# Optimization experiments

Measured on AMD Instinct MI355X. Metric: run time of the kernel, lower is better.

Reference implementation:

```python
import jax, jax.numpy as jnp
import numpy as np

# Mamba-1.4B-like dims
BATCH, SEQ, HID = 1, 2048, 2048
INTER, STATE, DT_RANK, KCONV = 4096, 16, 128, 4


def setup_inputs() -> dict:
    key = jax.random.key(0)
    ks = jax.random.split(key, 8)
    f = jnp.float32
    return {
        "input_states": jax.random.normal(ks[0], (BATCH, SEQ, HID), f),
        "in_proj_w": jax.random.normal(ks[1], (HID, 2 * INTER), f) * (HID ** -0.5),
        "conv_w": jax.random.normal(ks[2], (INTER, 1, KCONV), f) * (KCONV ** -0.5),  # (O, I/groups=1, K) depthwise
        "conv_b": jnp.zeros((INTER,), f),
        "x_proj_w": jax.random.normal(ks[3], (INTER, DT_RANK + 2 * STATE), f) * (INTER ** -0.5),
        "dt_proj_w": jax.random.normal(ks[4], (DT_RANK, INTER), f) * (DT_RANK ** -0.5),
        "dt_proj_b": jax.random.normal(ks[5], (INTER,), f) * 0.1,
        "A_log": jnp.log(jnp.broadcast_to(jnp.arange(1, STATE + 1, dtype=f), (INTER, STATE))),
        "D": jnp.ones((INTER,), f),
        "out_proj_w": jax.random.normal(ks[6], (INTER, HID), f) * (INTER ** -0.5),
    }


def _mamba_forward(input_states, in_proj_w, conv_w, conv_b, x_proj_w,
                   dt_proj_w, dt_proj_b, A_log, D, out_proj_w):
    Bsz, L, _ = input_states.shape
    Idim, _, K = conv_w.shape
    N = A_log.shape[1]
    R = dt_proj_w.shape[0]

    proj = input_states @ in_proj_w                       # (B, L, 2I)
    hidden, gate = jnp.split(proj, 2, axis=-1)            # each (B, L, I)

    # depthwise causal conv over sequence (pad K-1, keep first L outputs)
    xc = jnp.swapaxes(hidden, 1, 2)                       # (B, I, L)
    xc = jax.lax.conv_general_dilated(
        xc, conv_w, window_strides=(1,), padding=((K - 1, K - 1),),
        feature_group_count=Idim)
    xc = xc[:, :, :L] + conv_b[None, :, None]
    u = jax.nn.silu(jnp.swapaxes(xc, 1, 2))               # (B, L, I)

    # input-dependent SSM params
    ssm_in = u @ x_proj_w                                 # (B, L, R + 2N)
    dt_in, Bc, Cc = jnp.split(ssm_in, [R, R + N], axis=-1)
    dt = jax.nn.softplus(dt_in @ dt_proj_w + dt_proj_b)   # (B, L, I)
    A = -jnp.exp(A_log)                                   # (I, N)

    def step(state, xs):
        dt_t, B_t, C_t, u_t = xs                          # (B,I) (B,N) (B,N) (B,I)
        dA = jnp.exp(dt_t[:, :, None] * A[None])          # (B, I, N)
        state = state * dA + (dt_t * u_t)[:, :, None] * B_t[:, None, :]
        y_t = jnp.einsum('bin,bn->bi', state, C_t)
        return state, y_t

    xs = (jnp.swapaxes(dt, 0, 1), jnp.swapaxes(Bc, 0, 1),
          jnp.swapaxes(Cc, 0, 1), jnp.swapaxes(u, 0, 1))
    state0 = jnp.zeros((Bsz, Idim, N), dt.dtype)
    _, ys = jax.lax.scan(step, state0, xs)                # (L, B, I)
    y = jnp.swapaxes(ys, 0, 1)                            # (B, L, I)

    y = (y + u * D) * jax.nn.silu(gate)
    return y @ out_proj_w                                 # (B, L, H)


def reference(input_states, in_proj_w, conv_w, conv_b, x_proj_w,
              dt_proj_w, dt_proj_b, A_log, D, out_proj_w):
    return _mamba_forward(input_states, in_proj_w, conv_w, conv_b, x_proj_w,
                          dt_proj_w, dt_proj_b, A_log, D, out_proj_w)
```

## Files before the change

### kernel.cpp

```cpp
#include <hip/hip_runtime.h>
#include <stdint.h>

#define LSEQ 2048
#define HID  2048
#define IDIM 4096
#define NSTATE 16
#define RRANK 128
#define GDIM 160

#define GCHUNK 64
#define TCHUNK (LSEQ / GCHUNK)

typedef _Float16 f16x8 __attribute__((ext_vector_type(8)));
typedef _Float16 f16x2 __attribute__((ext_vector_type(2)));
typedef float f32x4 __attribute__((ext_vector_type(4)));

#define GLOAD_LDS16(g, l) __builtin_amdgcn_global_load_lds( \
    (const __attribute__((address_space(1))) void*)(g),     \
    (__attribute__((address_space(3))) void*)(l), 16, 0, 0)

__device__ __forceinline__ float softplus_f(float x) {
    if (x > 20.f) return x;
    return log1pf(__expf(x));
}
__device__ __forceinline__ float silu_f(float x) {
    return x / (1.f + __expf(-x));
}

__device__ __forceinline__ void transpose_tile(const float* __restrict__ in,
                                               _Float16* __restrict__ out,
                                               int R, int C, int tr, int tc,
                                               _Float16 (*tile)[66]) {
    const int c0 = tc * 64, r0 = tr * 64;
    const int t = threadIdx.x;
    const int tx = t & 15, ty = t >> 4;
    const int ox = t & 7, oy = t >> 3;
    const bool full = (c0 + 64 <= C) && (r0 + 64 <= R);
    if (full) {
        #pragma unroll
        for (int j = 0; j < 4; ++j) {
            int r = ty + j * 16;
            float4 v = *(const float4*)(in + (long)(r0 + r) * C + c0 + tx * 4);
            tile[r][tx * 4 + 0] = (_Float16)v.x;
            tile[r][tx * 4 + 1] = (_Float16)v.y;
            tile[r][tx * 4 + 2] = (_Float16)v.z;
            tile[r][tx * 4 + 3] = (_Float16)v.w;
        }
        __syncthreads();
        #pragma unroll
        for (int j = 0; j < 2; ++j) {
            int c = oy + j * 32;
            f16x8 v;
            #pragma unroll
            for (int e = 0; e < 8; ++e) v[e] = tile[ox * 8 + e][c];
            *(f16x8*)(out + (long)(c0 + c) * R + r0 + ox * 8) = v;
        }
    } else {
        #pragma unroll
        for (int j = 0; j < 4; ++j) {
            int r = ty + j * 16;
            #pragma unroll
            for (int e = 0; e < 4; ++e) {
                int c = c0 + tx * 4 + e;
                float v = (r0 + r < R && c < C) ? in[(long)(r0 + r) * C + c] : 0.f;
                tile[r][tx * 4 + e] = (_Float16)v;
            }
        }
        __syncthreads();
        #pragma unroll
        for (int j = 0; j < 2; ++j) {
            int c = c0 + oy + j * 32;
            if (c < C) {
                #pragma unroll
                for (int e = 0; e < 8; ++e) {
                    int r = r0 + ox * 8 + e;
                    if (r < R) out[(long)c * R + r] = tile[ox * 8 + e][oy + j * 32];
                }
            }
        }
    }
}

__global__ __launch_bounds__(256)
void prep_kernel(const float* __restrict__ x_in, const float* __restrict__ w_in,
                 const float* __restrict__ xw, const float* __restrict__ dtw,
                 const float* __restrict__ ow,
                 _Float16* __restrict__ Xf, _Float16* __restrict__ Wt1,
                 _Float16* __restrict__ Wt2, _Float16* __restrict__ Wt3,
                 _Float16* __restrict__ Wt4) {
    __shared__ _Float16 tile[64][66];
    int b = blockIdx.x;
    if (b < 4096) { transpose_tile(w_in, Wt1, HID, 2 * IDIM, b / 128, b % 128, tile); return; }
    b -= 4096;
    if (b < 192) { transpose_tile(xw, Wt2, IDIM, GDIM, b / 3, b % 3, tile); return; }
    b -= 192;
    if (b < 128) { transpose_tile(dtw, Wt3, RRANK, IDIM, b / 64, b % 64, tile); return; }
    b -= 128;
    if (b < 2048) { transpose_tile(ow, Wt4, IDIM, HID, b / 32, b % 32, tile); return; }
    b -= 2048;
    long base = (long)b * 4096 + threadIdx.x * 16;
    #pragma unroll
    for (int h = 0; h < 2; ++h) {
        float4 a = *(const float4*)(x_in + base + h * 8);
        float4 c = *(const float4*)(x_in + base + h * 8 + 4);
        f16x8 v;
        v[0] = (_Float16)a.x; v[1] = (_Float16)a.y; v[2] = (_Float16)a.z; v[3] = (_Float16)a.w;
        v[4] = (_Float16)c.x; v[5] = (_Float16)c.y; v[6] = (_Float16)c.z; v[7] = (_Float16)c.w;
        *(f16x8*)(Xf + base + h * 8) = v;
    }
}

#define BM 128
#define BK 64

template <typename CT, int BN_, bool SOFTPLUS>
__global__ __launch_bounds__(256)
void gemm_bt_kernel(const _Float16* __restrict__ A, const _Float16* __restrict__ Bt,
                    CT* __restrict__ C, int M, int N, int K, int kc,
                    const float* __restrict__ bias) {
    constexpr int NI = BN_ / 32;
    constexpr int NISS_B = BN_ * 8 / 256;
    __shared__ _Float16 As[BM * BK];
    __shared__ _Float16 Bs[BN_ * BK];
    const int m0 = blockIdx.y * BM;
    const int n0 = blockIdx.x * BN_;
    const int t = threadIdx.x;
    const int wave = t >> 6;
    const int lane = t & 63;
    const int wm = wave >> 1, wn = wave & 1;
    const int lrow = lane & 15;
    const int quad = lane >> 4;
    const int sw8 = (lrow & 7) * 8;

    f32x4 acc[4][NI];
    #pragma unroll
    for (int mi = 0; mi < 4; ++mi)
        #pragma unroll
        for (int ni = 0; ni < NI; ++ni)
            #pragma unroll
            for (int r = 0; r < 4; ++r)
                acc[mi][ni][r] = 0.f;

    const int k_begin = blockIdx.z * kc;
    const _Float16* pA[4];
    #pragma unroll
    for (int j = 0; j < 4; ++j) {
        int s = j * 256 + t;
        int row = s >> 3;
        int ch = (s & 7) ^ (row & 7);
        pA[j] = A + (long)(m0 + row) * K + ch * 8 + k_begin;
    }
    const _Float16* pB[NISS_B];
    #pragma unroll
    for (int j = 0; j < NISS_B; ++j) {
        int s = j * 256 + t;
        int row = s >> 3;
        int ch = (s & 7) ^ (row & 7);
        pB[j] = Bt + (long)(n0 + row) * K + ch * 8 + k_begin;
    }

    for (int kk = 0; kk < kc; kk += BK) {
        #pragma unroll
        for (int j = 0; j < 4; ++j) {
            GLOAD_LDS16(pA[j], As + (j * 256 + wave * 64) * 8);
            pA[j] += BK;
        }
        #pragma unroll
        for (int j = 0; j < NISS_B; ++j) {
            GLOAD_LDS16(pB[j], Bs + (j * 256 + wave * 64) * 8);
            pB[j] += BK;
        }
        __syncthreads();

        #pragma unroll
        for (int h = 0; h < 2; ++h) {
            const int qoff = (h * 32 + quad * 8) ^ sw8;
            f16x8 af[4], bf[NI];
            #pragma unroll
            for (int mi = 0; mi < 4; ++mi)
                af[mi] = *(const f16x8*)(As + (wm * 64 + mi * 16 + lrow) * BK + qoff);
            #pragma unroll
            for (int ni = 0; ni < NI; ++ni)
                bf[ni] = *(const f16x8*)(Bs + (wn * (BN_ / 2) + ni * 16 + lrow) * BK + qoff);
            #pragma unroll
            for (int mi = 0; mi < 4; ++mi)
                #pragma unroll
                for (int ni = 0; ni < NI; ++ni)
                    acc[mi][ni] = __builtin_amdgcn_mfma_f32_16x16x32_f16(af[mi], bf[ni], acc[mi][ni], 0, 0, 0);
        }
        __syncthreads();
    }

    CT* Cz = C + (long)blockIdx.z * M * N;
    #pragma unroll
    for (int mi = 0; mi < 4; ++mi) {
        #pragma unroll
        for (int ni = 0; ni < NI; ++ni) {
            int col = n0 + wn * (BN_ / 2) + ni * 16 + lrow;
            if (col < N) {
                float bv = SOFTPLUS ? bias[col] : 0.f;
                #pragma unroll
                for (int r = 0; r < 4; ++r) {
                    int row = m0 + wm * 64 + mi * 16 + quad * 4 + r;
                    float v = acc[mi][ni][r];
                    if (SOFTPLUS) v = softplus_f(v + bv);
                    Cz[(long)row * N + col] = (CT)v;
                }
            }
        }
    }
}

__global__ void xproj_reduce_kernel(const float* __restrict__ part, float* __restrict__ ssm,
                                    _Float16* __restrict__ dtin) {
    int idx = blockIdx.x * 256 + threadIdx.x;
    if (idx >= LSEQ * GDIM) return;
    int t = idx / GDIM;
    int c = idx - t * GDIM;
    float v = 0.f;
    #pragma unroll
    for (int k = 0; k < 8; ++k)
        v += part[((long)k * LSEQ + t) * 256 + c];
    ssm[idx] = v;
    if (c < RRANK) dtin[t * RRANK + c] = (_Float16)v;
}

__global__ void opart_reduce_kernel(const float* __restrict__ part, float* __restrict__ out) {
    int idx = blockIdx.x * 256 + threadIdx.x;
    float4 a = ((const float4*)part)[idx];
    float4 b = ((const float4*)(part + (long)LSEQ * HID))[idx];
    ((float4*)out)[idx] = make_float4(a.x + b.x, a.y + b.y, a.z + b.z, a.w + b.w);
}

__global__ void conv_silu_kernel(const _Float16* __restrict__ proj, const float* __restrict__ w,
                                 const float* __restrict__ b, _Float16* __restrict__ u16) {
    int idx = blockIdx.x * 256 + threadIdx.x;
    int i0 = (idx & 511) * 8;
    int t0 = (idx >> 9) * 4;
    f16x8 r[7];
    #pragma unroll
    for (int k = 0; k < 7; ++k) {
        int tt = t0 - 3 + k;
        if (tt >= 0) r[k] = *(const f16x8*)(proj + (long)tt * (2 * IDIM) + i0);
        else         r[k] = f16x8{0,0,0,0,0,0,0,0};
    }
    float4 wv[8]; float bb[8];
    #pragma unroll
    for (int j = 0; j < 8; ++j) { wv[j] = ((const float4*)w)[i0 + j]; bb[j] = b[i0 + j]; }
    #pragma unroll
    for (int tt = 0; tt < 4; ++tt) {
        f16x8 res;
        #pragma unroll
        for (int j = 0; j < 8; ++j) {
            float a = bb[j] + (float)r[tt][j] * wv[j].x + (float)r[tt+1][j] * wv[j].y
                            + (float)r[tt+2][j] * wv[j].z + (float)r[tt+3][j] * wv[j].w;
            res[j] = (_Float16)(a / (1.f + __expf(-a)));
        }
        *(f16x8*)(u16 + (long)(t0 + tt) * IDIM + i0) = res;
    }
}

__global__ __launch_bounds__(256)
void scan_pass1_kernel(const _Float16* __restrict__ dtf, const float* __restrict__ ssm,
                       const _Float16* __restrict__ u16, const float* __restrict__ A_log,
                       _Float16* __restrict__ Pc, _Float16* __restrict__ Sc) {
    const int c = blockIdx.y;
    const int i0 = (blockIdx.x * 256 + threadIdx.x) * 2;

    __shared__ float Bs[TCHUNK * 16];
    for (int idx = threadIdx.x; idx < TCHUNK * 16; idx += 256) {
        int t = idx >> 4, n = idx & 15;
        Bs[idx] = ssm[(c * TCHUNK + t) * GDIM + RRANK + n];
    }
    __syncthreads();

    float A[2][16];
    #pragma unroll
    for (int ch = 0; ch < 2; ++ch) {
        const float4* Ap = (const float4*)(A_log + (long)(i0 + ch) * 16);
        #pragma unroll
        for (int q = 0; q < 4; ++q) {
            float4 v = Ap[q];
            A[ch][q * 4 + 0] = -__expf(v.x);
            A[ch][q * 4 + 1] = -__expf(v.y);
            A[ch][q * 4 + 2] = -__expf(v.z);
            A[ch][q * 4 + 3] = -__expf(v.w);
        }
    }

    float s[2][16], pr[2][16];
    #pragma unroll
    for (int ch = 0; ch < 2; ++ch)
        #pragma unroll
        for (int n = 0; n < 16; ++n) { s[ch][n] = 0.f; pr[ch][n] = 1.f; }

    long base = (long)c * TCHUNK * IDIM + i0;
    for (int t = 0; t < TCHUNK; ++t) {
        f16x2 dt2 = *(const f16x2*)(dtf + base + (long)t * IDIM);
        f16x2 u2  = *(const f16x2*)(u16 + base + (long)t * IDIM);
        #pragma unroll
        for (int ch = 0; ch < 2; ++ch) {
            float dt = (float)dt2[ch];
            float dtu = dt * (float)u2[ch];
            #pragma unroll
            for (int n = 0; n < 16; ++n) {
                float dA = __expf(dt * A[ch][n]);
                s[ch][n] = s[ch][n] * dA + dtu * Bs[t * 16 + n];
                pr[ch][n] *= dA;
            }
        }
    }

    long o = ((long)c * IDIM + i0) * 16;
    #pragma unroll
    for (int ch = 0; ch < 2; ++ch) {
        #pragma unroll
        for (int q = 0; q < 2; ++q) {
            f16x8 pv, sv;
            #pragma unroll
            for (int e = 0; e < 8; ++e) {
                pv[e] = (_Float16)pr[ch][q * 8 + e];
                sv[e] = (_Float16)s[ch][q * 8 + e];
            }
            *(f16x8*)(Pc + o + ch * 16 + q * 8) = pv;
            *(f16x8*)(Sc + o + ch * 16 + q * 8) = sv;
        }
    }
}

__global__ void scan_combine_kernel(const _Float16* __restrict__ Pc, _Float16* __restrict__ ScInit) {
    int tid = blockIdx.x * 256 + threadIdx.x;
    const long stride = (long)IDIM * 16;
    const long off = (long)tid * 2;
    f16x2 p4[4], s4[4];
    #pragma unroll
    for (int k = 0; k < 4; ++k) {
        p4[k] = *(const f16x2*)(Pc + (long)k * stride + off);
        s4[k] = *(const f16x2*)(ScInit + (long)k * stride + off);
    }
    float c0 = 0.f, c1 = 0.f;
    for (int g = 0; g < GCHUNK / 4; ++g) {
        f16x2 pc[4], sc[4];
        #pragma unroll
        for (int k = 0; k < 4; ++k) { pc[k] = p4[k]; sc[k] = s4[k]; }
        if (g + 1 < GCHUNK / 4) {
            #pragma unroll
            for (int k = 0; k < 4; ++k) {
                long o2 = (long)((g + 1) * 4 + k) * stride + off;
                p4[k] = *(const f16x2*)(Pc + o2);
                s4[k] = *(const f16x2*)(ScInit + o2);
            }
        }
        #pragma unroll
        for (int k = 0; k < 4; ++k) {
            long o = (long)(g * 4 + k) * stride + off;
            *(f16x2*)(ScInit + o) = f16x2{(_Float16)c0, (_Float16)c1};
            c0 = c0 * (float)pc[k][0] + (float)sc[k][0];
            c1 = c1 * (float)pc[k][1] + (float)sc[k][1];
        }
    }
}

__global__ __launch_bounds__(256)
void scan_pass3_kernel(const _Float16* __restrict__ dtf, const float* __restrict__ ssm,
                       const _Float16* __restrict__ u16, const _Float16* __restrict__ proj,
                       const float* __restrict__ A_log, const float* __restrict__ Dp,
                       const _Float16* __restrict__ Init, _Float16* __restrict__ y16) {
    const int c = blockIdx.y;
    const int i0 = (blockIdx.x * 256 + threadIdx.x) * 2;

    __shared__ float Bs[TCHUNK * 16];
    __shared__ float Cs[TCHUNK * 16];
    for (int idx = threadIdx.x; idx < TCHUNK * 16; idx += 256) {
        int t = idx >> 4, n = idx & 15;
        Bs[idx] = ssm[(c * TCHUNK + t) * GDIM + RRANK + n];
        Cs[idx] = ssm[(c * TCHUNK + t) * GDIM + RRANK + NSTATE + n];
    }
    __syncthreads();

    float A[2][16];
    #pragma unroll
    for (int ch = 0; ch < 2; ++ch) {
        const float4* Ap = (const float4*)(A_log + (long)(i0 + ch) * 16);
        #pragma unroll
        for (int q = 0; q < 4; ++q) {
            float4 v = Ap[q];
            A[ch][q * 4 + 0] = -__expf(v.x);
            A[ch][q * 4 + 1] = -__expf(v.y);
            A[ch][q * 4 + 2] = -__expf(v.z);
            A[ch][q * 4 + 3] = -__expf(v.w);
        }
    }
    float2 Dv = *(const float2*)(Dp + i0);

    float s[2][16];
    {
        long o = ((long)c * IDIM + i0) * 16;
        #pragma unroll
        for (int ch = 0; ch < 2; ++ch)
            #pragma unroll
            for (int q = 0; q < 2; ++q) {
                f16x8 v = *(const f16x8*)(Init + o + ch * 16 + q * 8);
                #pragma unroll
                for (int e = 0; e < 8; ++e) s[ch][q * 8 + e] = (float)v[e];
            }
    }

    long base = (long)c * TCHUNK * IDIM + i0;
    for (int t = 0; t < TCHUNK; ++t) {
        f16x2 dt2 = *(const f16x2*)(dtf + base + (long)t * IDIM);
        f16x2 u2  = *(const f16x2*)(u16 + base + (long)t * IDIM);
        int tg = c * TCHUNK + t;
        f16x2 g2 = *(const f16x2*)(proj + (long)tg * (2 * IDIM) + IDIM + i0);
        f16x2 res;
        #pragma unroll
        for (int ch = 0; ch < 2; ++ch) {
            float dt = (float)dt2[ch];
            float uv = (float)u2[ch];
            float dtu = dt * uv;
            float y = 0.f;
            #pragma unroll
            for (int n = 0; n < 16; ++n) {
                float dA = __expf(dt * A[ch][n]);
                s[ch][n] = s[ch][n] * dA + dtu * Bs[t * 16 + n];
                y += s[ch][n] * Cs[t * 16 + n];
            }
            float g = (float)g2[ch];
            float Dch = ch ? Dv.y : Dv.x;
            res[ch] = (_Float16)((y + uv * Dch) * silu_f(g));
        }
        *(f16x2*)(y16 + base + (long)t * IDIM) = res;
    }
}

extern "C" void kernel_launch(void* const* d_in, const int* in_sizes, int n_in,
                              void* d_out, int out_size, void* d_ws, size_t ws_size,
                              hipStream_t stream) {
    const float* x_in  = (const float*)d_in[0];
    const float* w_in  = (const float*)d_in[1];
    const float* cw    = (const float*)d_in[2];
    const float* cb    = (const float*)d_in[3];
    const float* xw    = (const float*)d_in[4];
    const float* dtw   = (const float*)d_in[5];
    const float* dtb   = (const float*)d_in[6];
    const float* alog  = (const float*)d_in[7];
    const float* Dp    = (const float*)d_in[8];
    const float* ow    = (const float*)d_in[9];
    float* out = (float*)d_out;

    char* p = (char*)d_ws;
    auto alloc = [&](size_t bytes) { char* r = p; p += (bytes + 255) & ~255ull; return r; };
    _Float16* Xf    = (_Float16*)alloc((size_t)LSEQ * HID * 2);
    _Float16* Wt1   = (_Float16*)alloc((size_t)2 * IDIM * HID * 2);
    _Float16* proj  = (_Float16*)alloc((size_t)LSEQ * 2 * IDIM * 2);
    _Float16* u16   = (_Float16*)alloc((size_t)LSEQ * IDIM * 2);
    _Float16* Wt2   = (_Float16*)alloc((size_t)256 * IDIM * 2);
    float*    ssm   = (float*)alloc((size_t)LSEQ * GDIM * 4);
    _Float16* dtin  = (_Float16*)alloc((size_t)LSEQ * RRANK * 2);
    _Float16* Wt3   = (_Float16*)alloc((size_t)IDIM * RRANK * 2);
    _Float16* dtf   = (_Float16*)alloc((size_t)LSEQ * IDIM * 2);
    _Float16* Wt4   = (_Float16*)alloc((size_t)HID * IDIM * 2);
    _Float16* y16   = (_Float16*)alloc((size_t)LSEQ * IDIM * 2);

    float* xpart = (float*)Wt1;
    _Float16* Pc = (_Float16*)Wt1;
    _Float16* Sc = Pc + (size_t)GCHUNK * IDIM * 16;
    float* opart = (float*)Wt1;

    prep_kernel<<<7488, 256, 0, stream>>>(x_in, w_in, xw, dtw, ow, Xf, Wt1, Wt2, Wt3, Wt4);
    gemm_bt_kernel<_Float16, 128, false><<<dim3(2 * IDIM / 128, LSEQ / BM, 1), 256, 0, stream>>>(
        Xf, Wt1, proj, LSEQ, 2 * IDIM, HID, HID, nullptr);
    conv_silu_kernel<<<(LSEQ / 4) * (IDIM / 8) / 256, 256, 0, stream>>>(proj, cw, cb, u16);
    gemm_bt_kernel<float, 128, false><<<dim3(2, LSEQ / BM, 8), 256, 0, stream>>>(
        u16, Wt2, xpart, LSEQ, 256, IDIM, IDIM / 8, nullptr);
    xproj_reduce_kernel<<<(LSEQ * GDIM + 255) / 256, 256, 0, stream>>>(xpart, ssm, dtin);
    gemm_bt_kernel<_Float16, 128, true><<<dim3(IDIM / 128, LSEQ / BM, 1), 256, 0, stream>>>(
        dtin, Wt3, dtf, LSEQ, IDIM, RRANK, RRANK, dtb);
    scan_pass1_kernel<<<dim3(IDIM / 512, GCHUNK), 256, 0, stream>>>(
        dtf, ssm, u16, alog, Pc, Sc);
    scan_combine_kernel<<<(IDIM * NSTATE / 2) / 256, 256, 0, stream>>>(Pc, Sc);
    scan_pass3_kernel<<<dim3(IDIM / 512, GCHUNK), 256, 0, stream>>>(
        dtf, ssm, u16, proj, alog, Dp, Sc, y16);
    gemm_bt_kernel<float, 128, false><<<dim3(HID / 128, LSEQ / BM, 2), 256, 0, stream>>>(
        y16, Wt4, opart, LSEQ, HID, IDIM, IDIM / 2, nullptr);
    opart_reduce_kernel<<<(LSEQ * HID / 4) / 256, 256, 0, stream>>>(opart, out);
}
```

Measured before the change: 470.6 us.

## Overlap weight transposes with in-proj GEMM and trim scan/reduce traffic

Moves the x_proj, dt_proj and out_proj weight transposes out of the prep kernel and into the in-projection GEMM launch as extra blocks, so they run alongside the GEMM tiles. It also doubles the x_proj split-K factor, stores the out_proj split-K partials in fp16 with a vectorized reduce, and in scan pass 1 replaces the per-state running product of decays with a single exp of A times the summed dt. These changes aim to cut launch count, partial-sum traffic and exp/multiply work, at the cost of fp16 rounding on output partials and a larger x_proj reduction.

```diff
diff --git a/kernel.cpp b/kernel.cpp
--- a/kernel.cpp
+++ b/kernel.cpp
@@ -83,21 +83,11 @@
 
 __global__ __launch_bounds__(256)
 void prep_kernel(const float* __restrict__ x_in, const float* __restrict__ w_in,
-                 const float* __restrict__ xw, const float* __restrict__ dtw,
-                 const float* __restrict__ ow,
-                 _Float16* __restrict__ Xf, _Float16* __restrict__ Wt1,
-                 _Float16* __restrict__ Wt2, _Float16* __restrict__ Wt3,
-                 _Float16* __restrict__ Wt4) {
+                 _Float16* __restrict__ Xf, _Float16* __restrict__ Wt1) {
     __shared__ _Float16 tile[64][66];
     int b = blockIdx.x;
     if (b < 4096) { transpose_tile(w_in, Wt1, HID, 2 * IDIM, b / 128, b % 128, tile); return; }
     b -= 4096;
-    if (b < 192) { transpose_tile(xw, Wt2, IDIM, GDIM, b / 3, b % 3, tile); return; }
-    b -= 192;
-    if (b < 128) { transpose_tile(dtw, Wt3, RRANK, IDIM, b / 64, b % 64, tile); return; }
-    b -= 128;
-    if (b < 2048) { transpose_tile(ow, Wt4, IDIM, HID, b / 32, b % 32, tile); return; }
-    b -= 2048;
     long base = (long)b * 4096 + threadIdx.x * 16;
     #pragma unroll
     for (int h = 0; h < 2; ++h) {
@@ -113,17 +103,13 @@
 #define BM 128
 #define BK 64
 
-template <typename CT, int BN_, bool SOFTPLUS>
-__global__ __launch_bounds__(256)
-void gemm_bt_kernel(const _Float16* __restrict__ A, const _Float16* __restrict__ Bt,
-                    CT* __restrict__ C, int M, int N, int K, int kc,
-                    const float* __restrict__ bias) {
-    constexpr int NI = BN_ / 32;
-    constexpr int NISS_B = BN_ * 8 / 256;
-    __shared__ _Float16 As[BM * BK];
-    __shared__ _Float16 Bs[BN_ * BK];
-    const int m0 = blockIdx.y * BM;
-    const int n0 = blockIdx.x * BN_;
+template <typename CT, bool SOFTPLUS>
+__device__ __forceinline__
+void gemm_core(const _Float16* __restrict__ A, const _Float16* __restrict__ Bt,
+               CT* __restrict__ C, int M, int N, int K, int kc,
+               const float* __restrict__ bias,
+               _Float16* __restrict__ As, _Float16* __restrict__ Bs,
+               int m0, int n0, int zz) {
     const int t = threadIdx.x;
     const int wave = t >> 6;
     const int lane = t & 63;
@@ -132,30 +118,24 @@
     const int quad = lane >> 4;
     const int sw8 = (lrow & 7) * 8;
 
-    f32x4 acc[4][NI];
+    f32x4 acc[4][4];
     #pragma unroll
     for (int mi = 0; mi < 4; ++mi)
         #pragma unroll
-        for (int ni = 0; ni < NI; ++ni)
+        for (int ni = 0; ni < 4; ++ni)
             #pragma unroll
             for (int r = 0; r < 4; ++r)
                 acc[mi][ni][r] = 0.f;
 
-    const int k_begin = blockIdx.z * kc;
+    const int k_begin = zz * kc;
     const _Float16* pA[4];
+    const _Float16* pB[4];
     #pragma unroll
     for (int j = 0; j < 4; ++j) {
         int s = j * 256 + t;
         int row = s >> 3;
         int ch = (s & 7) ^ (row & 7);
         pA[j] = A + (long)(m0 + row) * K + ch * 8 + k_begin;
-    }
-    const _Float16* pB[NISS_B];
-    #pragma unroll
-    for (int j = 0; j < NISS_B; ++j) {
-        int s = j * 256 + t;
-        int row = s >> 3;
-        int ch = (s & 7) ^ (row & 7);
         pB[j] = Bt + (long)(n0 + row) * K + ch * 8 + k_begin;
     }
 
@@ -164,9 +144,6 @@
         for (int j = 0; j < 4; ++j) {
             GLOAD_LDS16(pA[j], As + (j * 256 + wave * 64) * 8);
             pA[j] += BK;
-        }
-        #pragma unroll
-        for (int j = 0; j < NISS_B; ++j) {
             GLOAD_LDS16(pB[j], Bs + (j * 256 + wave * 64) * 8);
             pB[j] += BK;
         }
@@ -175,28 +152,28 @@
         #pragma unroll
         for (int h = 0; h < 2; ++h) {
             const int qoff = (h * 32 + quad * 8) ^ sw8;
-            f16x8 af[4], bf[NI];
+            f16x8 af[4], bf[4];
             #pragma unroll
             for (int mi = 0; mi < 4; ++mi)
                 af[mi] = *(const f16x8*)(As + (wm * 64 + mi * 16 + lrow) * BK + qoff);
             #pragma unroll
-            for (int ni = 0; ni < NI; ++ni)
-                bf[ni] = *(const f16x8*)(Bs + (wn * (BN_ / 2) + ni * 16 + lrow) * BK + qoff);
+            for (int ni = 0; ni < 4; ++ni)
+                bf[ni] = *(const f16x8*)(Bs + (wn * 64 + ni * 16 + lrow) * BK + qoff);
             #pragma unroll
             for (int mi = 0; mi < 4; ++mi)
                 #pragma unroll
-                for (int ni = 0; ni < NI; ++ni)
+                for (int ni = 0; ni < 4; ++ni)
                     acc[mi][ni] = __builtin_amdgcn_mfma_f32_16x16x32_f16(af[mi], bf[ni], acc[mi][ni], 0, 0, 0);
         }
         __syncthreads();
     }
 
-    CT* Cz = C + (long)blockIdx.z * M * N;
+    CT* Cz = C + (long)zz * M * N;
     #pragma unroll
     for (int mi = 0; mi < 4; ++mi) {
         #pragma unroll
-        for (int ni = 0; ni < NI; ++ni) {
-            int col = n0 + wn * (BN_ / 2) + ni * 16 + lrow;
+        for (int ni = 0; ni < 4; ++ni) {
+            int col = n0 + wn * 64 + ni * 16 + lrow;
             if (col < N) {
                 float bv = SOFTPLUS ? bias[col] : 0.f;
                 #pragma unroll
@@ -211,6 +188,40 @@
     }
 }
 
+template <typename CT, bool SOFTPLUS>
+__global__ __launch_bounds__(256)
+void gemm_bt_kernel(const _Float16* __restrict__ A, const _Float16* __restrict__ Bt,
+                    CT* __restrict__ C, int M, int N, int K, int kc,
+                    const float* __restrict__ bias) {
+    __shared__ _Float16 As[BM * BK];
+    __shared__ _Float16 Bs[128 * BK];
+    gemm_core<CT, SOFTPLUS>(A, Bt, C, M, N, K, kc, bias, As, Bs,
+                            blockIdx.y * BM, blockIdx.x * 128, blockIdx.z);
+}
+
+__global__ __launch_bounds__(256)
+void inproj_plus_kernel(const _Float16* __restrict__ Xf, const _Float16* __restrict__ Wt1,
+                        _Float16* __restrict__ proj,
+                        const float* __restrict__ xw, const float* __restrict__ dtw,
+                        const float* __restrict__ ow,
+                        _Float16* __restrict__ Wt2, _Float16* __restrict__ Wt3,
+                        _Float16* __restrict__ Wt4) {
+    __shared__ _Float16 smem[BM * BK + 128 * BK];
+    int b = blockIdx.x;
+    if (b < 1024) {
+        gemm_core<_Float16, false>(Xf, Wt1, proj, LSEQ, 2 * IDIM, HID, HID, nullptr,
+                                   smem, smem + BM * BK, (b >> 6) * BM, (b & 63) * 128, 0);
+        return;
+    }
+    b -= 1024;
+    _Float16 (*tile)[66] = (_Float16 (*)[66])smem;
+    if (b < 192) { transpose_tile(xw, Wt2, IDIM, GDIM, b / 3, b % 3, tile); return; }
+    b -= 192;
+    if (b < 128) { transpose_tile(dtw, Wt3, RRANK, IDIM, b / 64, b % 64, tile); return; }
+    b -= 128;
+    transpose_tile(ow, Wt4, IDIM, HID, b / 32, b % 32, tile);
+}
+
 __global__ void xproj_reduce_kernel(const float* __restrict__ part, float* __restrict__ ssm,
                                     _Float16* __restrict__ dtin) {
     int idx = blockIdx.x * 256 + threadIdx.x;
@@ -219,17 +230,25 @@
     int c = idx - t * GDIM;
     float v = 0.f;
     #pragma unroll
-    for (int k = 0; k < 8; ++k)
+    for (int k = 0; k < 16; ++k)
         v += part[((long)k * LSEQ + t) * 256 + c];
     ssm[idx] = v;
     if (c < RRANK) dtin[t * RRANK + c] = (_Float16)v;
 }
 
-__global__ void opart_reduce_kernel(const float* __restrict__ part, float* __restrict__ out) {
-    int idx = blockIdx.x * 256 + threadIdx.x;
-    float4 a = ((const float4*)part)[idx];
-    float4 b = ((const float4*)(part + (long)LSEQ * HID))[idx];
-    ((float4*)out)[idx] = make_float4(a.x + b.x, a.y + b.y, a.z + b.z, a.w + b.w);
+__global__ void opart_reduce_kernel(const _Float16* __restrict__ part, float* __restrict__ out) {
+    long base = ((long)blockIdx.x * 256 + threadIdx.x) * 32;
+    #pragma unroll
+    for (int j = 0; j < 4; ++j) {
+        f16x8 a = *(const f16x8*)(part + base + j * 8);
+        f16x8 b = *(const f16x8*)(part + (long)LSEQ * HID + base + j * 8);
+        float4 o0 = make_float4((float)a[0] + (float)b[0], (float)a[1] + (float)b[1],
+                                (float)a[2] + (float)b[2], (float)a[3] + (float)b[3]);
+        float4 o1 = make_float4((float)a[4] + (float)b[4], (float)a[5] + (float)b[5],
+                                (float)a[6] + (float)b[6], (float)a[7] + (float)b[7]);
+        *(float4*)(out + base + j * 8) = o0;
+        *(float4*)(out + base + j * 8 + 4) = o1;
+    }
 }
 
 __global__ void conv_silu_kernel(const _Float16* __restrict__ proj, const float* __restrict__ w,
@@ -288,11 +307,12 @@
         }
     }
 
-    float s[2][16], pr[2][16];
+    float s[2][16];
+    float sumdt[2] = {0.f, 0.f};
     #pragma unroll
     for (int ch = 0; ch < 2; ++ch)
         #pragma unroll
-        for (int n = 0; n < 16; ++n) { s[ch][n] = 0.f; pr[ch][n] = 1.f; }
+        for (int n = 0; n < 16; ++n) s[ch][n] = 0.f;
 
     long base = (long)c * TCHUNK * IDIM + i0;
     for (int t = 0; t < TCHUNK; ++t) {
@@ -302,11 +322,11 @@
         for (int ch = 0; ch < 2; ++ch) {
             float dt = (float)dt2[ch];
             float dtu = dt * (float)u2[ch];
+            sumdt[ch] += dt;
             #pragma unroll
             for (int n = 0; n < 16; ++n) {
                 float dA = __expf(dt * A[ch][n]);
                 s[ch][n] = s[ch][n] * dA + dtu * Bs[t * 16 + n];
-                pr[ch][n] *= dA;
             }
         }
     }
@@ -319,7 +339,7 @@
             f16x8 pv, sv;
             #pragma unroll
             for (int e = 0; e < 8; ++e) {
-                pv[e] = (_Float16)pr[ch][q * 8 + e];
+                pv[e] = (_Float16)__expf(A[ch][q * 8 + e] * sumdt[ch]);
                 sv[e] = (_Float16)s[ch][q * 8 + e];
             }
             *(f16x8*)(Pc + o + ch * 16 + q * 8) = pv;
@@ -465,23 +485,23 @@
     float* xpart = (float*)Wt1;
     _Float16* Pc = (_Float16*)Wt1;
     _Float16* Sc = Pc + (size_t)GCHUNK * IDIM * 16;
-    float* opart = (float*)Wt1;
-
-    prep_kernel<<<7488, 256, 0, stream>>>(x_in, w_in, xw, dtw, ow, Xf, Wt1, Wt2, Wt3, Wt4);
-    gemm_bt_kernel<_Float16, 128, false><<<dim3(2 * IDIM / 128, LSEQ / BM, 1), 256, 0, stream>>>(
-        Xf, Wt1, proj, LSEQ, 2 * IDIM, HID, HID, nullptr);
+    _Float16* opart = (_Float16*)Wt1;
+
+    prep_kernel<<<5120, 256, 0, stream>>>(x_in, w_in, Xf, Wt1);
+    inproj_plus_kernel<<<1024 + 192 + 128 + 2048, 256, 0, stream>>>(
+        Xf, Wt1, proj, xw, dtw, ow, Wt2, Wt3, Wt4);
     conv_silu_kernel<<<(LSEQ / 4) * (IDIM / 8) / 256, 256, 0, stream>>>(proj, cw, cb, u16);
-    gemm_bt_kernel<float, 128, false><<<dim3(2, LSEQ / BM, 8), 256, 0, stream>>>(
-        u16, Wt2, xpart, LSEQ, 256, IDIM, IDIM / 8, nullptr);
+    gemm_bt_kernel<float, false><<<dim3(2, LSEQ / BM, 16), 256, 0, stream>>>(
+        u16, Wt2, xpart, LSEQ, 256, IDIM, IDIM / 16, nullptr);
     xproj_reduce_kernel<<<(LSEQ * GDIM + 255) / 256, 256, 0, stream>>>(xpart, ssm, dtin);
-    gemm_bt_kernel<_Float16, 128, true><<<dim3(IDIM / 128, LSEQ / BM, 1), 256, 0, stream>>>(
+    gemm_bt_kernel<_Float16, true><<<dim3(IDIM / 128, LSEQ / BM, 1), 256, 0, stream>>>(
         dtin, Wt3, dtf, LSEQ, IDIM, RRANK, RRANK, dtb);
     scan_pass1_kernel<<<dim3(IDIM / 512, GCHUNK), 256, 0, stream>>>(
         dtf, ssm, u16, alog, Pc, Sc);
     scan_combine_kernel<<<(IDIM * NSTATE / 2) / 256, 256, 0, stream>>>(Pc, Sc);
     scan_pass3_kernel<<<dim3(IDIM / 512, GCHUNK), 256, 0, stream>>>(
         dtf, ssm, u16, proj, alog, Dp, Sc, y16);
-    gemm_bt_kernel<float, 128, false><<<dim3(HID / 128, LSEQ / BM, 2), 256, 0, stream>>>(
+    gemm_bt_kernel<_Float16, false><<<dim3(HID / 128, LSEQ / BM, 2), 256, 0, stream>>>(
         y16, Wt4, opart, LSEQ, HID, IDIM, IDIM / 2, nullptr);
-    opart_reduce_kernel<<<(LSEQ * HID / 4) / 256, 256, 0, stream>>>(opart, out);
-}
+    opart_reduce_kernel<<<(LSEQ * HID / 32) / 256, 256, 0, stream>>>(opart, out);
+}
```

Measured after the change: 463.2 us. Within noise of the previous version (-1.6%).
